# Kernel tuning notes

Measured on AMD Instinct MI355X. Metric: run time of the kernel, lower is better.

The kernel has to match this reference:

```python
import jax, jax.numpy as jnp
import numpy as np

L, D, H, F_IN = 3, 256, 8, 5
HD = D // H
FF = 4 * D
EPS = 1e-5


def _layer_norm(x, g, b):
    mu = jnp.mean(x, axis=-1, keepdims=True)
    var = jnp.mean(jnp.square(x - mu), axis=-1, keepdims=True)
    return (x - mu) * jax.lax.rsqrt(var + EPS) * g + b


def setup_inputs() -> dict:
    key = jax.random.key(0)
    ks = jax.random.split(key, 20)
    s = 0.02
    inp = {
        'x': jax.random.normal(ks[0], (32, 512, F_IN), jnp.float32),
        'mask': jax.random.randint(ks[1], (32, 512), 0, 2) == 1,
        'Win': jax.random.normal(ks[2], (F_IN, D), jnp.float32) * s,
        'bin_': jnp.zeros((D,), jnp.float32),
        'Wq': jax.random.normal(ks[3], (L, D, D), jnp.float32) * s,
        'bq': jnp.zeros((L, D), jnp.float32),
        'Wk': jax.random.normal(ks[4], (L, D, D), jnp.float32) * s,
        'bk': jnp.zeros((L, D), jnp.float32),
        'Wv': jax.random.normal(ks[5], (L, D, D), jnp.float32) * s,
        'bv': jnp.zeros((L, D), jnp.float32),
        'Wo': jax.random.normal(ks[6], (L, D, D), jnp.float32) * s,
        'bo': jnp.zeros((L, D), jnp.float32),
        'g1': jnp.ones((L, D), jnp.float32),
        'b1': jnp.zeros((L, D), jnp.float32),
        'W1': jax.random.normal(ks[7], (L, D, FF), jnp.float32) * s,
        'c1': jnp.zeros((L, FF), jnp.float32),
        'W2': jax.random.normal(ks[8], (L, FF, D), jnp.float32) * s,
        'c2': jnp.zeros((L, D), jnp.float32),
        'g2': jnp.ones((L, D), jnp.float32),
        'b2': jnp.zeros((L, D), jnp.float32),
    }
    return inp


def reference(x, mask, Win, bin_, Wq, bq, Wk, bk, Wv, bv, Wo, bo, g1, b1, W1, c1, W2, c2, g2, b2):
    B, S, _ = x.shape
    scale = 1.0 / jnp.sqrt(jnp.float32(HD))
    h = x @ Win + bin_  # [B,S,D]
    kmask = mask[:, None, None, :]  # [B,1,1,S] key-padding mask
    for l in range(L):
        q = (h @ Wq[l] + bq[l]).reshape(B, S, H, HD).transpose(0, 2, 1, 3)
        k = (h @ Wk[l] + bk[l]).reshape(B, S, H, HD).transpose(0, 2, 1, 3)
        v = (h @ Wv[l] + bv[l]).reshape(B, S, H, HD).transpose(0, 2, 1, 3)
        scores = jnp.einsum('bhqd,bhkd->bhqk', q, k) * scale
        scores = jnp.where(kmask, -jnp.inf, scores)
        attn = jnp.nan_to_num(jax.nn.softmax(scores, axis=-1), nan=0.0)
        ao = jnp.einsum('bhqk,bhkd->bhqd', attn, v).transpose(0, 2, 1, 3).reshape(B, S, D)
        ao = ao @ Wo[l] + bo[l]
        h = _layer_norm(h + ao, g1[l], b1[l])
        ff = jax.nn.relu(h @ W1[l] + c1[l]) @ W2[l] + c2[l]
        h = _layer_norm(h + ff, g2[l], b2[l])
    return h
```

## Files before the change

kernel.cpp:

```cpp
#include <hip/hip_runtime.h>
#include <cstdint>

#define NLAYER 3
#define DMODEL 256
#define NHEAD 8
#define HEADD 32
#define FFDIM 1024
#define BATCH 32
#define SEQ 512
#define MTOK (BATCH*SEQ)

typedef __attribute__((ext_vector_type(8))) __bf16 bf16x8;
typedef __attribute__((ext_vector_type(4))) __bf16 bf16x4;
typedef __attribute__((ext_vector_type(4))) float f32x4;
typedef __attribute__((ext_vector_type(16))) float f32x16;

typedef __attribute__((address_space(1))) const uint8_t ga_t;
typedef __attribute__((address_space(3))) uint8_t la_t;
__device__ __forceinline__ void gll16(const void* g, void* l) {
    __builtin_amdgcn_global_load_lds((ga_t*)g, (la_t*)l, 16, 0, 0);
}

__global__ __launch_bounds__(256)
void prep_kernel(const float* __restrict__ Wq, const float* __restrict__ Wk,
                 const float* __restrict__ Wv, const float* __restrict__ Wo,
                 const float* __restrict__ W1, const float* __restrict__ W2,
                 const float* __restrict__ bq, const float* __restrict__ bk,
                 const float* __restrict__ bv,
                 __bf16* __restrict__ wqkv, __bf16* __restrict__ wot,
                 __bf16* __restrict__ w1t, __bf16* __restrict__ w2t,
                 float* __restrict__ bqkv,
                 const float* __restrict__ x, const float* __restrict__ Win,
                 const float* __restrict__ bin, __bf16* __restrict__ h16)
{
    const int bid = blockIdx.x;
    const int tid = threadIdx.x;
    if (bid >= 2313) {
        const int m0 = (bid - 2313) * 8;
        const float bv_ = bin[tid];
#pragma unroll
        for (int p = 0; p < 8; ++p) {
            const int m = m0 + p;
            const float* xr = x + (size_t)m * 5;
            float acc = bv_;
#pragma unroll
            for (int k = 0; k < 5; ++k) acc += xr[k] * Win[k * DMODEL + tid];
            h16[(size_t)m * DMODEL + tid] = (__bf16)acc;
        }
        return;
    }
    if (bid >= 3 * 768) {
        int idx = (bid - 3 * 768) * 256 + tid;
        int l = idx / 768, j = idx % 768;
        float v = (j < 256) ? bq[l * 256 + j]
                : (j < 512) ? bk[l * 256 + j - 256]
                            : bv[l * 256 + j - 512];
        bqkv[idx] = v;
        return;
    }
    const int l = bid / 768;
    const int rr = bid % 768;
    const float* src; __bf16* dst; int K, N, t;
    if (rr < 192) {
        int ty = rr >> 6; t = rr & 63;
        src = (ty == 0 ? Wq : ty == 1 ? Wk : Wv) + (size_t)l * 65536;
        dst = wqkv + (size_t)l * 768 * 256 + (size_t)ty * 65536;
        K = 256; N = 256;
    } else if (rr < 256) {
        t = rr - 192; src = Wo + (size_t)l * 65536; dst = wot + (size_t)l * 65536;
        K = 256; N = 256;
    } else if (rr < 512) {
        t = rr - 256; src = W1 + (size_t)l * 262144; dst = w1t + (size_t)l * 262144;
        K = 256; N = 1024;
    } else {
        t = rr - 512; src = W2 + (size_t)l * 262144; dst = w2t + (size_t)l * 262144;
        K = 1024; N = 256;
    }
    const int tn = N >> 5;
    const int tk = t / tn, tj = t % tn;
    __shared__ float tile[32][33];
    const int c = tid & 31, rbase = tid >> 5;
#pragma unroll
    for (int p = 0; p < 4; ++p) {
        int kr = rbase + p * 8;
        tile[kr][c] = src[(size_t)(tk * 32 + kr) * N + tj * 32 + c];
    }
    __syncthreads();
#pragma unroll
    for (int p = 0; p < 4; ++p) {
        int nr = rbase + p * 8;
        dst[(size_t)(tj * 32 + nr) * K + tk * 32 + c] = (__bf16)tile[c][nr];
    }
}

template<int RELU>
__global__ __launch_bounds__(256, 2)
void gemm_kernel(const __bf16* __restrict__ A, const __bf16* __restrict__ Bt,
                 const float* __restrict__ bias,
                 __bf16* __restrict__ C, int N)
{
    __shared__ __bf16 Bs[128 * 256];
    __shared__ __bf16 As[2][64 * 64];
    const int tid = threadIdx.x;
    const int m0 = blockIdx.x * 128;
    const int n0 = blockIdx.y * 128;
    const int lane = tid & 63;
    const int wave = tid >> 6;
    const int wm = (wave & 1) * 64;
    const int wn = (wave >> 1) * 64;
    const int fr = lane & 15;
    const int quad = lane >> 4;

    {
        const int rsub = lane >> 5;
#pragma unroll
        for (int c = 0; c < 16; ++c) {
            const int rl = wave * 32 + c * 2 + rsub;
            const int g = ((lane & 31) - 4 * rl) & 31;
            gll16(Bt + (size_t)(n0 + rl) * 256 + g * 8,
                  Bs + (wave * 32 + c * 2) * 256);
        }
    }
    const int arow8 = lane >> 3;
    const int apos = lane & 7;
#define STAGE_A(ks, buf)                                                      \
    {                                                                         \
        _Pragma("unroll")                                                     \
        for (int s_ = 0; s_ < 2; ++s_) {                                      \
            const int c_ = wave * 2 + s_;                                     \
            const int row_ = c_ * 8 + arow8;                                  \
            const int g_ = apos ^ (row_ & 7);                                 \
            gll16(A + (size_t)(m0 + row_ + 64 * (g_ >> 2)) * 256              \
                    + (ks) * 32 + (g_ & 3) * 8,                               \
                  &As[buf][c_ * 8 * 64]);                                     \
        }                                                                     \
    }
    STAGE_A(0, 0);
    __syncthreads();

    f32x4 acc[4][4];
#pragma unroll
    for (int i = 0; i < 4; ++i)
#pragma unroll
        for (int j = 0; j < 4; ++j)
#pragma unroll
            for (int r = 0; r < 4; ++r) acc[i][j][r] = 0.f;

    const int aposr = ((wave & 1) * 4 + quad) ^ (fr & 7);

#pragma unroll
    for (int ks = 0; ks < 8; ++ks) {
        if (ks < 7) STAGE_A(ks + 1, (ks + 1) & 1);
        const __bf16* Ab = As[ks & 1];
        bf16x8 af[4], bfr[4];
#pragma unroll
        for (int i = 0; i < 4; ++i) {
            const int row = i * 16 + fr;
            af[i] = *(const bf16x8*)(Ab + row * 64 + aposr * 8);
        }
#pragma unroll
        for (int j = 0; j < 4; ++j) {
            const int row = wn + j * 16 + fr;
            const int pos = (ks * 4 + quad + 4 * fr) & 31;
            bfr[j] = *(const bf16x8*)(Bs + row * 256 + pos * 8);
        }
#pragma unroll
        for (int i = 0; i < 4; ++i)
#pragma unroll
            for (int j = 0; j < 4; ++j)
                acc[i][j] = __builtin_amdgcn_mfma_f32_16x16x32_bf16(
                    af[i], bfr[j], acc[i][j], 0, 0, 0);
        __syncthreads();
    }
#undef STAGE_A

#pragma unroll
    for (int i = 0; i < 4; ++i) {
#pragma unroll
        for (int j = 0; j < 4; ++j) {
            const int gc = n0 + wn + j * 16 + fr;
            const float bv = bias[gc];
#pragma unroll
            for (int r = 0; r < 4; ++r) {
                const int gr = m0 + wm + i * 16 + quad * 4 + r;
                float v = acc[i][j][r] + bv;
                if (RELU) v = fmaxf(v, 0.f);
                C[(size_t)gr * N + gc] = (__bf16)v;
            }
        }
    }
}

template<int LAST>
__global__ __launch_bounds__(256, 4)
void gemm_ln_kernel(const __bf16* __restrict__ A, const __bf16* __restrict__ Bt,
                    const float* __restrict__ bias, const __bf16* __restrict__ res,
                    const float* __restrict__ g, const float* __restrict__ be,
                    __bf16* __restrict__ out16, float* __restrict__ out32, int K)
{
    __shared__ __bf16 As[32 * 64];
    __shared__ __bf16 Bs[256 * 64];
    __shared__ float red[32 * 8];
    const int tid = threadIdx.x;
    const int m0 = blockIdx.x * 32;
    const int lane = tid & 63;
    const int wave = tid >> 6;
    const int wn = wave * 64;
    const int fr = lane & 15;
    const int quad = lane >> 4;
    const int lr = lane >> 3;
    const int qg = (lane & 7) ^ lr;
    const int frs = fr & 7;

    const __bf16* Ab = A  + (size_t)(m0 + wave * 8 + lr) * K + qg * 8;
    const __bf16* Bb = Bt + (size_t)(wave * 64 + lr) * K + qg * 8;

    f32x4 acc[2][4];
#pragma unroll
    for (int i = 0; i < 2; ++i)
#pragma unroll
        for (int j = 0; j < 4; ++j)
#pragma unroll
            for (int r = 0; r < 4; ++r) acc[i][j][r] = 0.f;

    for (int k0 = 0; k0 < K; k0 += 64) {
        gll16(Ab + k0, As + wave * 512);
#pragma unroll
        for (int p = 0; p < 8; ++p)
            gll16(Bb + (size_t)p * 8 * K + k0, Bs + (wave * 8 + p) * 512);
        __syncthreads();
#pragma unroll
        for (int kk = 0; kk < 2; ++kk) {
            bf16x8 af[2], bfr[4];
#pragma unroll
            for (int i = 0; i < 2; ++i) {
                int row = i * 16 + fr;
                af[i] = *(const bf16x8*)(As + row * 64 + (((kk * 4 + quad) ^ frs) * 8));
            }
#pragma unroll
            for (int j = 0; j < 4; ++j) {
                int row = wn + j * 16 + fr;
                bfr[j] = *(const bf16x8*)(Bs + row * 64 + (((kk * 4 + quad) ^ frs) * 8));
            }
#pragma unroll
            for (int i = 0; i < 2; ++i)
#pragma unroll
                for (int j = 0; j < 4; ++j)
                    acc[i][j] = __builtin_amdgcn_mfma_f32_16x16x32_bf16(
                        af[i], bfr[j], acc[i][j], 0, 0, 0);
        }
        __syncthreads();
    }

    float bv[4];
#pragma unroll
    for (int j = 0; j < 4; ++j) bv[j] = bias[wn + j * 16 + fr];

#pragma unroll
    for (int i = 0; i < 2; ++i) {
#pragma unroll
        for (int r = 0; r < 4; ++r) {
            const int row = i * 16 + quad * 4 + r;
            float ps = 0.f, pq = 0.f;
#pragma unroll
            for (int j = 0; j < 4; ++j) {
                const int gc = wn + j * 16 + fr;
                float v = acc[i][j][r] + bv[j]
                        + (float)res[(size_t)(m0 + row) * DMODEL + gc];
                acc[i][j][r] = v;
                ps += v;
                pq += v * v;
            }
#pragma unroll
            for (int off = 1; off < 16; off <<= 1) {
                ps += __shfl_xor(ps, off, 64);
                pq += __shfl_xor(pq, off, 64);
            }
            if (fr == 0) {
                red[row * 8 + wave * 2]     = ps;
                red[row * 8 + wave * 2 + 1] = pq;
            }
        }
    }
    __syncthreads();

#pragma unroll
    for (int i = 0; i < 2; ++i) {
#pragma unroll
        for (int r = 0; r < 4; ++r) {
            const int row = i * 16 + quad * 4 + r;
            f32x4 a = *(const f32x4*)(red + row * 8);
            f32x4 b2 = *(const f32x4*)(red + row * 8 + 4);
            const float s  = a[0] + a[2] + b2[0] + b2[2];
            const float sq = a[1] + a[3] + b2[1] + b2[3];
            const float mu = s * (1.f / DMODEL);
            const float var = sq * (1.f / DMODEL) - mu * mu;
            const float rs = rsqrtf(var + 1e-5f);
#pragma unroll
            for (int j = 0; j < 4; ++j) {
                const int gc = wn + j * 16 + fr;
                float y = (acc[i][j][r] - mu) * rs * g[gc] + be[gc];
                if (LAST) out32[(size_t)(m0 + row) * DMODEL + gc] = y;
                else      out16[(size_t)(m0 + row) * DMODEL + gc] = (__bf16)y;
            }
        }
    }
}

__global__ __launch_bounds__(1024)
void attn_kernel(const __bf16* __restrict__ qkv, const int* __restrict__ mask,
                 __bf16* __restrict__ ao)
{
    __shared__ __bf16 Ks[512 * 40];
    __shared__ __bf16 Vt[32 * 520];
    __shared__ __bf16 Pq[16 * 32 * 40];
    __shared__ float maskadd[512];

    const int b = blockIdx.x >> 3;
    const int h = blockIdx.x & 7;
    const int t = threadIdx.x;
    const int lane = t & 63;
    const int wave = t >> 6;
    const int cl = lane & 31;
    const int kh = lane >> 5;
    const float scale = 0.17677669529663687f;

    const size_t base = (size_t)b * SEQ * 768;

#pragma unroll
    for (int p = 0; p < 2; ++p) {
        int idx = p * 1024 + t;
        int key = idx >> 2, ch = idx & 3;
        bf16x8 kv = *(const bf16x8*)(qkv + base + (size_t)key * 768 + 256 + h * 32 + ch * 8);
        *(bf16x8*)(Ks + key * 40 + ch * 8) = kv;
        bf16x8 vv = *(const bf16x8*)(qkv + base + (size_t)key * 768 + 512 + h * 32 + ch * 8);
#pragma unroll
        for (int j = 0; j < 8; ++j) Vt[(ch * 8 + j) * 520 + key] = vv[j];
    }
    if (t < 512) maskadd[t] = mask[b * SEQ + t] ? -1e30f : 0.f;
    __syncthreads();

    const int q0 = wave * 32;
    const __bf16* qrow = qkv + base + (size_t)(q0 + cl) * 768 + h * 32;
    bf16x8 qf0 = *(const bf16x8*)(qrow + kh * 8);
    bf16x8 qf1 = *(const bf16x8*)(qrow + 16 + kh * 8);

    f32x16 oacc;
#pragma unroll
    for (int i = 0; i < 16; ++i) oacc[i] = 0.f;
    float lsum = 0.f;
    __bf16* Pw = Pq + wave * 32 * 40;

    for (int kt = 0; kt < SEQ; kt += 32) {
        bf16x8 kf0 = *(const bf16x8*)(Ks + (kt + cl) * 40 + kh * 8);
        bf16x8 kf1 = *(const bf16x8*)(Ks + (kt + cl) * 40 + 16 + kh * 8);
        f32x16 s;
#pragma unroll
        for (int i = 0; i < 16; ++i) s[i] = 0.f;
        s = __builtin_amdgcn_mfma_f32_32x32x16_bf16(kf0, qf0, s, 0, 0, 0);
        s = __builtin_amdgcn_mfma_f32_32x32x16_bf16(kf1, qf1, s, 0, 0, 0);
        float pv[16];
#pragma unroll
        for (int g = 0; g < 4; ++g) {
            f32x4 mv = *(const f32x4*)(maskadd + kt + 8 * g + 4 * kh);
#pragma unroll
            for (int r = 0; r < 4; ++r) {
                float e = __expf(s[g * 4 + r] * scale + mv[r]);
                pv[g * 4 + r] = e;
                lsum += e;
            }
        }
#pragma unroll
        for (int g = 0; g < 4; ++g) {
            bf16x4 pb;
#pragma unroll
            for (int r = 0; r < 4; ++r) pb[r] = (__bf16)pv[g * 4 + r];
            *(bf16x4*)(Pw + cl * 40 + 8 * g + 4 * kh) = pb;
        }
        bf16x8 pf0 = *(const bf16x8*)(Pw + cl * 40 + kh * 8);
        bf16x8 pf1 = *(const bf16x8*)(Pw + cl * 40 + 16 + kh * 8);
        bf16x8 vf0 = *(const bf16x8*)(Vt + cl * 520 + kt + kh * 8);
        bf16x8 vf1 = *(const bf16x8*)(Vt + cl * 520 + kt + 16 + kh * 8);
        oacc = __builtin_amdgcn_mfma_f32_32x32x16_bf16(vf0, pf0, oacc, 0, 0, 0);
        oacc = __builtin_amdgcn_mfma_f32_32x32x16_bf16(vf1, pf1, oacc, 0, 0, 0);
    }

    lsum += __shfl_xor(lsum, 32);
    const float inv = (lsum > 0.f) ? 1.f / lsum : 0.f;
    __bf16* orow = ao + (size_t)(b * SEQ + q0 + cl) * DMODEL + h * 32;
#pragma unroll
    for (int g = 0; g < 4; ++g) {
        bf16x4 w;
#pragma unroll
        for (int r = 0; r < 4; ++r) w[r] = (__bf16)(oacc[g * 4 + r] * inv);
        *(bf16x4*)(orow + 8 * g + 4 * kh) = w;
    }
}

extern "C" void kernel_launch(void* const* d_in, const int* in_sizes, int n_in,
                              void* d_out, int out_size, void* d_ws, size_t ws_size,
                              hipStream_t stream)
{
    const float* x   = (const float*)d_in[0];
    const int*   mask= (const int*)d_in[1];
    const float* Win = (const float*)d_in[2];
    const float* bin = (const float*)d_in[3];
    const float* Wq  = (const float*)d_in[4];
    const float* bq  = (const float*)d_in[5];
    const float* Wk  = (const float*)d_in[6];
    const float* bk  = (const float*)d_in[7];
    const float* Wv  = (const float*)d_in[8];
    const float* bv  = (const float*)d_in[9];
    const float* Wo  = (const float*)d_in[10];
    const float* bo  = (const float*)d_in[11];
    const float* g1  = (const float*)d_in[12];
    const float* b1  = (const float*)d_in[13];
    const float* W1  = (const float*)d_in[14];
    const float* c1  = (const float*)d_in[15];
    const float* W2  = (const float*)d_in[16];
    const float* c2  = (const float*)d_in[17];
    const float* g2  = (const float*)d_in[18];
    const float* b2  = (const float*)d_in[19];

    char* ws = (char*)d_ws;
    size_t off = 0;
    auto alloc = [&](size_t bytes) -> void* {
        void* p = ws + off;
        off += (bytes + 255) & ~(size_t)255;
        return p;
    };
    __bf16* hA   = (__bf16*)alloc((size_t)MTOK * 256 * 2);
    __bf16* hB   = (__bf16*)alloc((size_t)MTOK * 256 * 2);
    __bf16* u    = (__bf16*)alloc((size_t)MTOK * 1024 * 2);
    __bf16* qkv  = u;
    __bf16* ffT  = u;
    __bf16* ao   = (__bf16*)alloc((size_t)MTOK * 256 * 2);
    __bf16* wqkv = (__bf16*)alloc((size_t)3 * 768 * 256 * 2);
    __bf16* wot  = (__bf16*)alloc((size_t)3 * 256 * 256 * 2);
    __bf16* w1t  = (__bf16*)alloc((size_t)3 * 1024 * 256 * 2);
    __bf16* w2t  = (__bf16*)alloc((size_t)3 * 256 * 1024 * 2);
    float*  bqkv = (float*)alloc((size_t)3 * 768 * 4);

    prep_kernel<<<dim3(2313 + MTOK / 8), dim3(256), 0, stream>>>(
        Wq, Wk, Wv, Wo, W1, W2, bq, bk, bv, wqkv, wot, w1t, w2t, bqkv,
        x, Win, bin, hA);

    for (int l = 0; l < NLAYER; ++l) {
        gemm_kernel<0><<<dim3(128, 6), dim3(256), 0, stream>>>(
            hA, wqkv + (size_t)l * 768 * 256, bqkv + l * 768, qkv, 768);
        attn_kernel<<<dim3(256), dim3(1024), 0, stream>>>(qkv, mask, ao);
        gemm_ln_kernel<0><<<dim3(MTOK / 32), dim3(256), 0, stream>>>(
            ao, wot + (size_t)l * 65536, bo + l * 256, hA,
            g1 + l * 256, b1 + l * 256, hB, nullptr, 256);
        gemm_kernel<1><<<dim3(128, 8), dim3(256), 0, stream>>>(
            hB, w1t + (size_t)l * 262144, c1 + l * 1024, ffT, 1024);
        if (l == 2) {
            gemm_ln_kernel<1><<<dim3(MTOK / 32), dim3(256), 0, stream>>>(
                ffT, w2t + (size_t)l * 262144, c2 + l * 256, hB,
                g2 + l * 256, b2 + l * 256, nullptr, (float*)d_out, 1024);
        } else {
            gemm_ln_kernel<0><<<dim3(MTOK / 32), dim3(256), 0, stream>>>(
                ffT, w2t + (size_t)l * 262144, c2 + l * 256, hB,
                g2 + l * 256, b2 + l * 256, hA, nullptr, 1024);
        }
    }
}
```

Baseline: 367.7 us.

## Fuse FFN up-projection, ReLU, down-projection and LayerNorm into one kernel

Replaces the separate W1 GEMM (writing a 16K x 1024 bf16 intermediate) and the W2 GEMM+LN with a single ff_kernel. It processes 32 rows per block in 128-column chunks and keeps the ReLU activations in LDS. Weights W1/W2 are pre-swizzled in the prep kernel into an MFMA-fragment layout so B operands load straight from global memory with coalesced 16-byte loads. This removes the HBM round trip of the FFN intermediate and one launch per layer. In exchange, every block rereads all FFN weights (served from L2), the grid is only 512 small blocks, and there is a sync per chunk.

```diff
diff --git a/kernel.cpp b/kernel.cpp
--- a/kernel.cpp
+++ b/kernel.cpp
@@ -28,7 +28,7 @@
                  const float* __restrict__ bq, const float* __restrict__ bk,
                  const float* __restrict__ bv,
                  __bf16* __restrict__ wqkv, __bf16* __restrict__ wot,
-                 __bf16* __restrict__ w1t, __bf16* __restrict__ w2t,
+                 __bf16* __restrict__ w1f, __bf16* __restrict__ w2f,
                  float* __restrict__ bqkv,
                  const float* __restrict__ x, const float* __restrict__ Win,
                  const float* __restrict__ bin, __bf16* __restrict__ h16)
@@ -60,36 +60,52 @@
     }
     const int l = bid / 768;
     const int rr = bid % 768;
-    const float* src; __bf16* dst; int K, N, t;
-    if (rr < 192) {
-        int ty = rr >> 6; t = rr & 63;
-        src = (ty == 0 ? Wq : ty == 1 ? Wk : Wv) + (size_t)l * 65536;
-        dst = wqkv + (size_t)l * 768 * 256 + (size_t)ty * 65536;
-        K = 256; N = 256;
-    } else if (rr < 256) {
-        t = rr - 192; src = Wo + (size_t)l * 65536; dst = wot + (size_t)l * 65536;
-        K = 256; N = 256;
-    } else if (rr < 512) {
-        t = rr - 256; src = W1 + (size_t)l * 262144; dst = w1t + (size_t)l * 262144;
-        K = 256; N = 1024;
-    } else {
-        t = rr - 512; src = W2 + (size_t)l * 262144; dst = w2t + (size_t)l * 262144;
-        K = 1024; N = 256;
-    }
+    __shared__ float tile[32][33];
+    const int c = tid & 31, rbase = tid >> 5;
+
+    if (rr < 256) {
+        const float* src; __bf16* dst; int t;
+        if (rr < 192) {
+            int ty = rr >> 6; t = rr & 63;
+            src = (ty == 0 ? Wq : ty == 1 ? Wk : Wv) + (size_t)l * 65536;
+            dst = wqkv + (size_t)l * 768 * 256 + (size_t)ty * 65536;
+        } else {
+            t = rr - 192; src = Wo + (size_t)l * 65536; dst = wot + (size_t)l * 65536;
+        }
+        const int tk = t >> 3, tj = t & 7;
+#pragma unroll
+        for (int p = 0; p < 4; ++p) {
+            int kr = rbase + p * 8;
+            tile[kr][c] = src[(size_t)(tk * 32 + kr) * 256 + tj * 32 + c];
+        }
+        __syncthreads();
+#pragma unroll
+        for (int p = 0; p < 4; ++p) {
+            int nr = rbase + p * 8;
+            dst[(size_t)(tj * 32 + nr) * 256 + tk * 32 + c] = (__bf16)tile[c][nr];
+        }
+        return;
+    }
+    const float* src; __bf16* dst; int N, KT, t;
+    if (rr < 512) { t = rr - 256; src = W1 + (size_t)l * 262144;
+                    dst = w1f + (size_t)l * 262144; N = 1024; KT = 8; }
+    else          { t = rr - 512; src = W2 + (size_t)l * 262144;
+                    dst = w2f + (size_t)l * 262144; N = 256;  KT = 32; }
     const int tn = N >> 5;
     const int tk = t / tn, tj = t % tn;
-    __shared__ float tile[32][33];
-    const int c = tid & 31, rbase = tid >> 5;
 #pragma unroll
     for (int p = 0; p < 4; ++p) {
         int kr = rbase + p * 8;
         tile[kr][c] = src[(size_t)(tk * 32 + kr) * N + tj * 32 + c];
     }
     __syncthreads();
-#pragma unroll
-    for (int p = 0; p < 4; ++p) {
-        int nr = rbase + p * 8;
-        dst[(size_t)(tj * 32 + nr) * K + tk * 32 + c] = (__bf16)tile[c][nr];
+    if (tid < 128) {
+        const int l_n = tid >> 2, k8 = tid & 3;
+        const int n = tj * 32 + l_n;
+        bf16x8 v;
+#pragma unroll
+        for (int j = 0; j < 8; ++j) v[j] = (__bf16)tile[k8 * 8 + j][l_n];
+        *(bf16x8*)(dst + ((size_t)((n >> 4) * KT + tk) * 64 + k8 * 16 + (n & 15)) * 8) = v;
     }
 }
 
@@ -300,6 +316,165 @@
             for (int j = 0; j < 4; ++j) {
                 const int gc = wn + j * 16 + fr;
                 float y = (acc[i][j][r] - mu) * rs * g[gc] + be[gc];
+                if (LAST) out32[(size_t)(m0 + row) * DMODEL + gc] = y;
+                else      out16[(size_t)(m0 + row) * DMODEL + gc] = (__bf16)y;
+            }
+        }
+    }
+}
+
+template<int LAST>
+__global__ __launch_bounds__(256, 3)
+void ff_kernel(const __bf16* __restrict__ A, const __bf16* __restrict__ w1f,
+               const float* __restrict__ c1, const __bf16* __restrict__ w2f,
+               const float* __restrict__ c2, const __bf16* __restrict__ res,
+               const float* __restrict__ g, const float* __restrict__ be,
+               __bf16* __restrict__ out16, float* __restrict__ out32)
+{
+    __shared__ __attribute__((aligned(16))) __bf16 As[4][32 * 64];
+    __shared__ __attribute__((aligned(16))) __bf16 P[32 * 136];
+    __shared__ float c1s[1024];
+    __shared__ float red[32 * 8];
+    const int tid = threadIdx.x;
+    const int lane = tid & 63;
+    const int wave = tid >> 6;
+    const int fr = lane & 15;
+    const int quad = lane >> 4;
+    const int m0 = blockIdx.x * 32;
+    const int frs = fr & 7;
+
+    {
+        const int lr = lane >> 3, pos = lane & 7;
+#pragma unroll
+        for (int c4 = 0; c4 < 4; ++c4) {
+            const int row = c4 * 8 + lr;
+            const int gsw = pos ^ (row & 7);
+            gll16(A + (size_t)(m0 + row) * 256 + wave * 64 + gsw * 8,
+                  &As[wave][c4 * 8 * 64]);
+        }
+    }
+    *(f32x4*)(c1s + tid * 4) = *(const f32x4*)(c1 + tid * 4);
+
+    f32x4 acc2[2][4];
+#pragma unroll
+    for (int i = 0; i < 2; ++i)
+#pragma unroll
+        for (int j = 0; j < 4; ++j)
+#pragma unroll
+            for (int r = 0; r < 4; ++r) acc2[i][j][r] = 0.f;
+    __syncthreads();
+
+    for (int ch = 0; ch < 8; ++ch) {
+        f32x4 acc1[2][2];
+#pragma unroll
+        for (int i = 0; i < 2; ++i)
+#pragma unroll
+            for (int j = 0; j < 2; ++j)
+#pragma unroll
+                for (int r = 0; r < 4; ++r) acc1[i][j][r] = 0.f;
+#pragma unroll
+        for (int ks = 0; ks < 8; ++ks) {
+            bf16x8 af[2], bfr[2];
+#pragma unroll
+            for (int i = 0; i < 2; ++i)
+                af[i] = *(const bf16x8*)(&As[ks >> 1][(i * 16 + fr) * 64
+                         + ((((ks & 1) * 4 + quad) ^ frs) * 8)]);
+#pragma unroll
+            for (int j = 0; j < 2; ++j) {
+                const int ntf = ch * 8 + wave * 2 + j;
+                bfr[j] = *(const bf16x8*)(w1f + ((size_t)(ntf * 8 + ks) * 64 + lane) * 8);
+            }
+#pragma unroll
+            for (int i = 0; i < 2; ++i)
+#pragma unroll
+                for (int j = 0; j < 2; ++j)
+                    acc1[i][j] = __builtin_amdgcn_mfma_f32_16x16x32_bf16(
+                        af[i], bfr[j], acc1[i][j], 0, 0, 0);
+        }
+#pragma unroll
+        for (int j = 0; j < 2; ++j) {
+            const float cb = c1s[ch * 128 + wave * 32 + j * 16 + fr];
+#pragma unroll
+            for (int i = 0; i < 2; ++i)
+#pragma unroll
+                for (int r = 0; r < 4; ++r) {
+                    const int rowm = i * 16 + quad * 4 + r;
+                    float v = fmaxf(acc1[i][j][r] + cb, 0.f);
+                    P[rowm * 136 + wave * 32 + j * 16 + fr] = (__bf16)v;
+                }
+        }
+        __syncthreads();
+#pragma unroll
+        for (int ks = 0; ks < 4; ++ks) {
+            bf16x8 pf[2], wf[4];
+#pragma unroll
+            for (int i = 0; i < 2; ++i)
+                pf[i] = *(const bf16x8*)(P + (i * 16 + fr) * 136 + ks * 32 + quad * 8);
+#pragma unroll
+            for (int j = 0; j < 4; ++j) {
+                const int ntg = wave * 4 + j;
+                const int kt = ch * 4 + ks;
+                wf[j] = *(const bf16x8*)(w2f + ((size_t)(ntg * 32 + kt) * 64 + lane) * 8);
+            }
+#pragma unroll
+            for (int i = 0; i < 2; ++i)
+#pragma unroll
+                for (int j = 0; j < 4; ++j)
+                    acc2[i][j] = __builtin_amdgcn_mfma_f32_16x16x32_bf16(
+                        pf[i], wf[j], acc2[i][j], 0, 0, 0);
+        }
+        __syncthreads();
+    }
+
+    const int wn = wave * 64;
+    float bv[4];
+#pragma unroll
+    for (int j = 0; j < 4; ++j) bv[j] = c2[wn + j * 16 + fr];
+
+#pragma unroll
+    for (int i = 0; i < 2; ++i) {
+#pragma unroll
+        for (int r = 0; r < 4; ++r) {
+            const int row = i * 16 + quad * 4 + r;
+            float ps = 0.f, pq = 0.f;
+#pragma unroll
+            for (int j = 0; j < 4; ++j) {
+                const int gc = wn + j * 16 + fr;
+                float v = acc2[i][j][r] + bv[j]
+                        + (float)res[(size_t)(m0 + row) * DMODEL + gc];
+                acc2[i][j][r] = v;
+                ps += v;
+                pq += v * v;
+            }
+#pragma unroll
+            for (int off = 1; off < 16; off <<= 1) {
+                ps += __shfl_xor(ps, off, 64);
+                pq += __shfl_xor(pq, off, 64);
+            }
+            if (fr == 0) {
+                red[row * 8 + wave * 2]     = ps;
+                red[row * 8 + wave * 2 + 1] = pq;
+            }
+        }
+    }
+    __syncthreads();
+
+#pragma unroll
+    for (int i = 0; i < 2; ++i) {
+#pragma unroll
+        for (int r = 0; r < 4; ++r) {
+            const int row = i * 16 + quad * 4 + r;
+            f32x4 a = *(const f32x4*)(red + row * 8);
+            f32x4 b2 = *(const f32x4*)(red + row * 8 + 4);
+            const float s  = a[0] + a[2] + b2[0] + b2[2];
+            const float sq = a[1] + a[3] + b2[1] + b2[3];
+            const float mu = s * (1.f / DMODEL);
+            const float var = sq * (1.f / DMODEL) - mu * mu;
+            const float rs = rsqrtf(var + 1e-5f);
+#pragma unroll
+            for (int j = 0; j < 4; ++j) {
+                const int gc = wn + j * 16 + fr;
+                float y = (acc2[i][j][r] - mu) * rs * g[gc] + be[gc];
                 if (LAST) out32[(size_t)(m0 + row) * DMODEL + gc] = y;
                 else      out16[(size_t)(m0 + row) * DMODEL + gc] = (__bf16)y;
             }
@@ -431,18 +606,16 @@
     };
     __bf16* hA   = (__bf16*)alloc((size_t)MTOK * 256 * 2);
     __bf16* hB   = (__bf16*)alloc((size_t)MTOK * 256 * 2);
-    __bf16* u    = (__bf16*)alloc((size_t)MTOK * 1024 * 2);
-    __bf16* qkv  = u;
-    __bf16* ffT  = u;
+    __bf16* qkv  = (__bf16*)alloc((size_t)MTOK * 768 * 2);
     __bf16* ao   = (__bf16*)alloc((size_t)MTOK * 256 * 2);
     __bf16* wqkv = (__bf16*)alloc((size_t)3 * 768 * 256 * 2);
     __bf16* wot  = (__bf16*)alloc((size_t)3 * 256 * 256 * 2);
-    __bf16* w1t  = (__bf16*)alloc((size_t)3 * 1024 * 256 * 2);
-    __bf16* w2t  = (__bf16*)alloc((size_t)3 * 256 * 1024 * 2);
+    __bf16* w1f  = (__bf16*)alloc((size_t)3 * 1024 * 256 * 2);
+    __bf16* w2f  = (__bf16*)alloc((size_t)3 * 256 * 1024 * 2);
     float*  bqkv = (float*)alloc((size_t)3 * 768 * 4);
 
     prep_kernel<<<dim3(2313 + MTOK / 8), dim3(256), 0, stream>>>(
-        Wq, Wk, Wv, Wo, W1, W2, bq, bk, bv, wqkv, wot, w1t, w2t, bqkv,
+        Wq, Wk, Wv, Wo, W1, W2, bq, bk, bv, wqkv, wot, w1f, w2f, bqkv,
         x, Win, bin, hA);
 
     for (int l = 0; l < NLAYER; ++l) {
@@ -452,16 +625,16 @@
         gemm_ln_kernel<0><<<dim3(MTOK / 32), dim3(256), 0, stream>>>(
             ao, wot + (size_t)l * 65536, bo + l * 256, hA,
             g1 + l * 256, b1 + l * 256, hB, nullptr, 256);
-        gemm_kernel<1><<<dim3(128, 8), dim3(256), 0, stream>>>(
-            hB, w1t + (size_t)l * 262144, c1 + l * 1024, ffT, 1024);
         if (l == 2) {
-            gemm_ln_kernel<1><<<dim3(MTOK / 32), dim3(256), 0, stream>>>(
-                ffT, w2t + (size_t)l * 262144, c2 + l * 256, hB,
-                g2 + l * 256, b2 + l * 256, nullptr, (float*)d_out, 1024);
+            ff_kernel<1><<<dim3(MTOK / 32), dim3(256), 0, stream>>>(
+                hB, w1f + (size_t)l * 262144, c1 + l * 1024,
+                w2f + (size_t)l * 262144, c2 + l * 256, hB,
+                g2 + l * 256, b2 + l * 256, nullptr, (float*)d_out);
         } else {
-            gemm_ln_kernel<0><<<dim3(MTOK / 32), dim3(256), 0, stream>>>(
-                ffT, w2t + (size_t)l * 262144, c2 + l * 256, hB,
-                g2 + l * 256, b2 + l * 256, hA, nullptr, 1024);
+            ff_kernel<0><<<dim3(MTOK / 32), dim3(256), 0, stream>>>(
+                hB, w1f + (size_t)l * 262144, c1 + l * 1024,
+                w2f + (size_t)l * 262144, c2 + l * 256, hB,
+                g2 + l * 256, b2 + l * 256, hA, nullptr);
         }
     }
 }
```

New measurement: 359.7 us. 1.02x faster.
